# Kernel tuning notes

Hardware: AMD Instinct MI355X
Metric: run time of the kernel (lower is better)

The kernel has to match this reference:

```python
import jax, jax.numpy as jnp
import numpy as np

B = 1024       # batch of graphs
NUM = 512      # predicates / nodes per graph
D = 64         # embedding_dim
H = 64         # hidden_dim
E = 4096       # edges per graph (shared structure across batch)
MAIN_NUM = 10  # softmax segment [0, MAIN_NUM); sigmoid on the rest


def setup_inputs() -> dict:
    key = jax.random.key(0)
    ks = jax.random.split(key, 8)
    x = jax.random.uniform(ks[0], (B, NUM), dtype=jnp.float32)
    embedding = jax.random.normal(ks[1], (NUM, D), dtype=jnp.float32) * 0.1
    W1 = jax.random.normal(ks[2], (D, H), dtype=jnp.float32) * (1.0 / np.sqrt(D))
    b1 = jnp.zeros((H,), jnp.float32)
    W2 = jax.random.normal(ks[3], (H, H), dtype=jnp.float32) * (1.0 / np.sqrt(H))
    b2 = jnp.zeros((H,), jnp.float32)
    W3 = jax.random.normal(ks[4], (H, 1), dtype=jnp.float32) * (1.0 / np.sqrt(H))
    b3 = jnp.zeros((1,), jnp.float32)
    edge_row = jax.random.randint(ks[5], (E,), 0, NUM, dtype=jnp.int32)
    edge_col = jax.random.randint(ks[6], (E,), 0, NUM, dtype=jnp.int32)
    return {"x": x, "embedding": embedding, "W1": W1, "b1": b1,
            "W2": W2, "b2": b2, "W3": W3, "b3": b3,
            "edge_row": edge_row, "edge_col": edge_col}


def _gcn_layer(h, W, b, row, col, norm):
    # h: [B, NUM, in]; GCNConv = linear -> D^{-1/2} A D^{-1/2} aggregate -> +bias
    hW = jnp.einsum('bni,io->bno', h, W)                 # [B, NUM, out]
    msg = hW[:, row, :] * norm[None, :, None]            # [B, E, out]
    agg = jnp.zeros_like(hW).at[:, col, :].add(msg)      # scatter to targets
    return agg + b


def reference(x, embedding, W1, b1, W2, b2, W3, b3, edge_row, edge_col):
    num = x.shape[1]
    # symmetric GCN normalization (add_self_loops=False, unit edge weights)
    deg = jnp.zeros((num,), x.dtype).at[edge_col].add(1.0)
    dinv = jnp.where(deg > 0, jax.lax.rsqrt(jnp.maximum(deg, 1.0)), 0.0)
    norm = dinv[edge_row] * dinv[edge_col]               # [E]

    h = x[..., None] * embedding                         # [B, NUM, D]
    h = jax.nn.relu(_gcn_layer(h, W1, b1, edge_row, edge_col, norm))
    h = jax.nn.relu(_gcn_layer(h, W2, b2, edge_row, edge_col, norm))
    logits = _gcn_layer(h, W3, b3, edge_row, edge_col, norm)[..., 0]  # [B, NUM]

    # convert_to_confidence: softmax over multiclass segment, sigmoid elsewhere
    phi_sm = jax.nn.softmax(logits[:, :MAIN_NUM], axis=1)
    phi_sg = jax.nn.sigmoid(logits[:, MAIN_NUM:])
    return jnp.concatenate([phi_sm, phi_sg], axis=1)
```

## Files before the change

kernel.cpp:

```cpp
#include <hip/hip_runtime.h>
#include <stdint.h>

#define NB    1024
#define NUM   512
#define HD    64
#define NE    4096
#define NEP   4608
#define MAIN  10
#define HBS   72

typedef __attribute__((ext_vector_type(8))) short short8;
typedef __attribute__((ext_vector_type(4))) float f32x4;

__device__ __forceinline__ short f2bf(float f) {
    uint32_t u = __float_as_uint(f);
    u += 0x7fffu + ((u >> 16) & 1u);
    return (short)(u >> 16);
}
__device__ __forceinline__ float bf2f(short s) {
    return __uint_as_float(((uint32_t)(uint16_t)s) << 16);
}

__global__ __launch_bounds__(512) void prep_all(
    const int* __restrict__ erow, const int* __restrict__ ecol,
    const float* __restrict__ emb, const float* __restrict__ W1,
    const float* __restrict__ W2,
    int* __restrict__ rsptr, int* __restrict__ colmap, int* __restrict__ epk,
    short* __restrict__ E1, short* __restrict__ W2T)
{
    const int t = threadIdx.x;
    if (blockIdx.x != 0) {
        int g = (blockIdx.x - 1) * 512 + t;
        if (g < NUM * HD) {
            int node = g >> 6, dim = g & 63;
            float acc = 0.0f;
            #pragma unroll
            for (int k = 0; k < HD; ++k) acc += emb[node * HD + k] * W1[k * HD + dim];
            E1[g] = f2bf(acc);
        } else if (g < NUM * HD + HD * HD) {
            int j = g - NUM * HD;
            int dout = j >> 6, din = j & 63;
            W2T[j] = f2bf(W2[din * HD + dout]);
        }
        return;
    }

    __shared__ int   sdeg[NUM];
    __shared__ int   aux[NUM];
    __shared__ float sdv[NUM];
    __shared__ int   rnk[NUM];
    __shared__ int   rdg[NUM];
    __shared__ int   wsum[8];

    const int lane = t & 63, wv = t >> 6;

    sdeg[t] = 0; aux[t] = 0;
    __syncthreads();
    for (int e = t; e < NE; e += 512) atomicAdd(&sdeg[ecol[e]], 1);
    __syncthreads();
    const int deg  = sdeg[t];
    const int pdeg = (deg + 1) & ~1;
    const int dbin = deg < NUM ? deg : NUM - 1;
    sdv[t] = deg > 0 ? rsqrtf((float)deg) : 0.0f;
    atomicAdd(&aux[dbin], 1);
    __syncthreads();
    {
        int v = aux[t];
        #pragma unroll
        for (int ofs = 1; ofs < 64; ofs <<= 1) {
            int sh = __shfl_up(v, ofs, 64);
            if (lane >= ofs) v += sh;
        }
        if (lane == 63) wsum[wv] = v;
        __syncthreads();
        if (t == 0) {
            int s = 0;
            #pragma unroll
            for (int w = 0; w < 8; ++w) { int tmp = wsum[w]; wsum[w] = s; s += tmp; }
        }
        __syncthreads();
        int inc = v + wsum[wv];
        sdeg[t] = inc - ((dbin == t) ? 0 : 0);
        aux[t]  = inc;
        __syncthreads();
        sdeg[t] = (t == 0) ? 0 : aux[t - 1];
        __syncthreads();
    }
    {
        int r = atomicAdd(&sdeg[dbin], 1);
        rnk[t] = r;
        rdg[r] = pdeg;
        colmap[r] = t;
    }
    __syncthreads();
    {
        int dv = rdg[t], v = dv;
        #pragma unroll
        for (int ofs = 1; ofs < 64; ofs <<= 1) {
            int sh = __shfl_up(v, ofs, 64);
            if (lane >= ofs) v += sh;
        }
        if (lane == 63) wsum[wv] = v;
        __syncthreads();
        if (t == 0) {
            int s = 0;
            #pragma unroll
            for (int w = 0; w < 8; ++w) { int tmp = wsum[w]; wsum[w] = s; s += tmp; }
        }
        __syncthreads();
        int inc  = v + wsum[wv];
        int excl = inc - dv;
        rsptr[t] = excl;
        if (t == NUM - 1) rsptr[NUM] = inc;
        aux[t] = excl;
        __syncthreads();
    }
    sdeg[t] = aux[rnk[t]];
    __syncthreads();
    for (int i = t; i < NEP; i += 512) epk[i] = 0;
    __syncthreads();
    for (int e = t; e < NE; e += 512) {
        int c = ecol[e], rr = erow[e];
        int p = atomicAdd(&sdeg[c], 1);
        unsigned nb = (unsigned short)f2bf(sdv[rr] * sdv[c]);
        epk[p] = (rr << 16) | (int)nb;
    }
}

__global__ __launch_bounds__(1024, 4) void gcn_body(
    const float* __restrict__ x, const short* __restrict__ E1,
    const short* __restrict__ W2T,
    const float* __restrict__ b1, const float* __restrict__ b2,
    const float* __restrict__ W3, const float* __restrict__ b3,
    const int* __restrict__ rsptrg, const int* __restrict__ colmap,
    const int* __restrict__ epkg,
    float* __restrict__ out)
{
    __shared__ short HA[NUM * HD];
    __shared__ short HB[NUM * HBS];
    __shared__ int   eps[NEP];
    __shared__ int   sptr[513];
    __shared__ float sred[2];

    float* tv   = (float*)HB;
    float* slog = ((float*)HB) + NUM;

    const int t     = threadIdx.x;
    const int b     = blockIdx.x;
    const int lane  = t & 63;
    const int wave  = t >> 6;
    const int q     = lane >> 4;
    const int l15   = lane & 15;
    const int grp   = lane >> 3;
    const int dbase = (lane & 7) * 8;

    {
        const int4* g4 = (const int4*)epkg;
        *(int4*)&eps[t * 4] = g4[t];
        if (t < 128) *(int4*)&eps[4096 + t * 4] = g4[1024 + t];
    }
    if (t < 513) sptr[t] = rsptrg[t];

    #pragma unroll
    for (int p = 0; p < 4; ++p) {
        int i = t + p * 1024;
        int r = i >> 3, d8 = (i & 7) * 8;
        float xr = x[b * NUM + r];
        short8 e = *(const short8*)&E1[r * HD + d8];
        short8 o;
        #pragma unroll
        for (int j = 0; j < 8; ++j) o[j] = f2bf(xr * bf2f(e[j]));
        *(short8*)&HA[r * HD + d8] = o;
    }

    float b1v[8], b2v[8], w3v[8];
    {
        f32x4 u0 = *(const f32x4*)&b1[dbase], u1 = *(const f32x4*)&b1[dbase + 4];
        f32x4 v0 = *(const f32x4*)&b2[dbase], v1 = *(const f32x4*)&b2[dbase + 4];
        f32x4 w0 = *(const f32x4*)&W3[dbase], w1 = *(const f32x4*)&W3[dbase + 4];
        #pragma unroll
        for (int j = 0; j < 4; ++j) {
            b1v[j] = u0[j]; b1v[j + 4] = u1[j];
            b2v[j] = v0[j]; b2v[j + 4] = v1[j];
            w3v[j] = w0[j]; w3v[j + 4] = w1[j];
        }
    }
    __syncthreads();

#define EDGE_MAC(pe)                                                          \
    {                                                                         \
        float n = __uint_as_float((unsigned)(pe) << 16);                      \
        uint4 hv = *(const uint4*)&HA[((unsigned)(pe) >> 16) * HD + dbase];   \
        a[0] = fmaf(n, __uint_as_float(hv.x << 16), a[0]);                    \
        a[1] = fmaf(n, __uint_as_float(hv.x), a[1]);                          \
        a[2] = fmaf(n, __uint_as_float(hv.y << 16), a[2]);                    \
        a[3] = fmaf(n, __uint_as_float(hv.y), a[3]);                          \
        a[4] = fmaf(n, __uint_as_float(hv.z << 16), a[4]);                    \
        a[5] = fmaf(n, __uint_as_float(hv.z), a[5]);                          \
        a[6] = fmaf(n, __uint_as_float(hv.w << 16), a[6]);                    \
        a[7] = fmaf(n, __uint_as_float(hv.w), a[7]);                          \
    }

    #pragma unroll 1
    for (int set = 0; set < 4; ++set) {
        int r  = set * 128 + wave * 8 + grp;
        int e0 = sptr[r], e1 = sptr[r + 1];
        int c  = colmap[r];
        float a[8];
        #pragma unroll
        for (int j = 0; j < 8; ++j) a[j] = 0.0f;
        int e = e0;
        for (; e + 4 <= e1; e += 4) {
            int2 pa = *(const int2*)&eps[e];
            int2 pb = *(const int2*)&eps[e + 2];
            EDGE_MAC(pa.x); EDGE_MAC(pa.y); EDGE_MAC(pb.x); EDGE_MAC(pb.y);
        }
        if (e < e1) {
            int2 pa = *(const int2*)&eps[e];
            EDGE_MAC(pa.x); EDGE_MAC(pa.y);
        }
        short8 o;
        #pragma unroll
        for (int j = 0; j < 8; ++j) o[j] = f2bf(fmaxf(a[j] + b1v[j], 0.0f));
        *(short8*)&HB[c * HBS + dbase] = o;
    }
    __syncthreads();

    {
        short8 bfr[2][4];
        #pragma unroll
        for (int ks = 0; ks < 2; ++ks)
            #pragma unroll
            for (int nt = 0; nt < 4; ++nt)
                bfr[ks][nt] = *(const short8*)&W2T[(nt * 16 + l15) * HD + ks * 32 + q * 8];
        f32x4 acc[2][4];
        #pragma unroll
        for (int mt = 0; mt < 2; ++mt)
            #pragma unroll
            for (int nt = 0; nt < 4; ++nt) acc[mt][nt] = (f32x4){0.f, 0.f, 0.f, 0.f};
        const int mbase = wave * 32;
        #pragma unroll
        for (int mt = 0; mt < 2; ++mt)
            #pragma unroll
            for (int ks = 0; ks < 2; ++ks) {
                short8 af = *(const short8*)&HB[(mbase + mt * 16 + l15) * HBS
                                                + ks * 32 + q * 8];
                #pragma unroll
                for (int nt = 0; nt < 4; ++nt)
                    acc[mt][nt] = __builtin_amdgcn_mfma_f32_16x16x32_bf16(
                        af, bfr[ks][nt], acc[mt][nt], 0, 0, 0);
            }
        #pragma unroll
        for (int mt = 0; mt < 2; ++mt)
            #pragma unroll
            for (int nt = 0; nt < 4; ++nt)
                #pragma unroll
                for (int i = 0; i < 4; ++i)
                    HA[(mbase + mt * 16 + q * 4 + i) * HD + nt * 16 + l15] =
                        f2bf(acc[mt][nt][i]);
    }
    __syncthreads();

    #pragma unroll 1
    for (int set = 0; set < 4; ++set) {
        int r  = set * 128 + wave * 8 + grp;
        int e0 = sptr[r], e1 = sptr[r + 1];
        int c  = colmap[r];
        float a[8];
        #pragma unroll
        for (int j = 0; j < 8; ++j) a[j] = 0.0f;
        int e = e0;
        for (; e + 4 <= e1; e += 4) {
            int2 pa = *(const int2*)&eps[e];
            int2 pb = *(const int2*)&eps[e + 2];
            EDGE_MAC(pa.x); EDGE_MAC(pa.y); EDGE_MAC(pb.x); EDGE_MAC(pb.y);
        }
        if (e < e1) {
            int2 pa = *(const int2*)&eps[e];
            EDGE_MAC(pa.x); EDGE_MAC(pa.y);
        }
        float v = 0.0f;
        #pragma unroll
        for (int j = 0; j < 8; ++j)
            v += fmaxf(a[j] + b2v[j], 0.0f) * w3v[j];
        v += __shfl_xor(v, 1, 64);
        v += __shfl_xor(v, 2, 64);
        v += __shfl_xor(v, 4, 64);
        if ((lane & 7) == 0) tv[c] = v;
    }
    __syncthreads();

    if (t < NUM) {
        int e0 = sptr[t], e1 = sptr[t + 1];
        float a = 0.0f;
        for (int e = e0; e < e1; ++e) {
            unsigned pe = (unsigned)eps[e];
            a = fmaf(__uint_as_float(pe << 16), tv[pe >> 16], a);
        }
        slog[colmap[t]] = a + b3[0];
    }
    __syncthreads();

    if (t < 64) {
        float v = (t < MAIN) ? slog[t] : -1e30f;
        float m = v;
        m = fmaxf(m, __shfl_xor(m, 1, 64));
        m = fmaxf(m, __shfl_xor(m, 2, 64));
        m = fmaxf(m, __shfl_xor(m, 4, 64));
        m = fmaxf(m, __shfl_xor(m, 8, 64));
        float ev = (t < MAIN) ? __expf(v - m) : 0.0f;
        ev += __shfl_xor(ev, 1, 64);
        ev += __shfl_xor(ev, 2, 64);
        ev += __shfl_xor(ev, 4, 64);
        ev += __shfl_xor(ev, 8, 64);
        if (t == 0) { sred[0] = m; sred[1] = ev; }
    }
    __syncthreads();

    if (t < NUM) {
        float l = slog[t];
        float o = (t < MAIN) ? __expf(l - sred[0]) / sred[1]
                             : 1.0f / (1.0f + __expf(-l));
        out[b * NUM + t] = o;
    }
#undef EDGE_MAC
}

extern "C" void kernel_launch(void* const* d_in, const int* in_sizes, int n_in,
                              void* d_out, int out_size, void* d_ws, size_t ws_size,
                              hipStream_t stream) {
    const float* x    = (const float*)d_in[0];
    const float* emb  = (const float*)d_in[1];
    const float* W1   = (const float*)d_in[2];
    const float* b1   = (const float*)d_in[3];
    const float* W2   = (const float*)d_in[4];
    const float* b2   = (const float*)d_in[5];
    const float* W3   = (const float*)d_in[6];
    const float* b3   = (const float*)d_in[7];
    const int*   erow = (const int*)d_in[8];
    const int*   ecol = (const int*)d_in[9];

    char* ws = (char*)d_ws;
    int*   rsptr  = (int*)ws;
    int*   colmap = (int*)(ws + 2176);
    int*   epk    = (int*)(ws + 4224);
    short* E1     = (short*)(ws + 22656);
    short* W2T    = (short*)(ws + 88192);

    prep_all<<<73, 512, 0, stream>>>(erow, ecol, emb, W1, W2,
                                     rsptr, colmap, epk, E1, W2T);
    gcn_body<<<NB, 1024, 0, stream>>>(x, E1, W2T, b1, b2, W3, b3,
                                      rsptr, colmap, epk, (float*)d_out);
}
```

Baseline: 157.3 us.

## Switch bf16 to fp16 storage, pre-shift edge indices, unroll gathers, split final aggregation

Changes intermediate storage and MFMA inputs from bf16 to fp16, and packs each edge's source row as a pre-scaled byte offset so the gather address needs only a shift. The edge-gather loops are unrolled to eight edges, with all row loads issued before the FMAs to raise LDS memory-level parallelism. The final scalar aggregation now uses two threads per node with a shuffle reduction. The fp16 conversions use round-toward-zero packing, which trades some accuracy and range for cheaper conversion. Some redundant prep code is also removed.

```diff
diff --git a/kernel.cpp b/kernel.cpp
--- a/kernel.cpp
+++ b/kernel.cpp
@@ -9,16 +9,14 @@
 #define MAIN  10
 #define HBS   72
 
-typedef __attribute__((ext_vector_type(8))) short short8;
+typedef _Float16 hlf;
+typedef __attribute__((ext_vector_type(2))) _Float16 hlf2;
+typedef __attribute__((ext_vector_type(8))) _Float16 hlf8;
 typedef __attribute__((ext_vector_type(4))) float f32x4;
 
-__device__ __forceinline__ short f2bf(float f) {
-    uint32_t u = __float_as_uint(f);
-    u += 0x7fffu + ((u >> 16) & 1u);
-    return (short)(u >> 16);
-}
-__device__ __forceinline__ float bf2f(short s) {
-    return __uint_as_float(((uint32_t)(uint16_t)s) << 16);
+__device__ __forceinline__ unsigned short f2h(float f) {
+    hlf v = (hlf)f;
+    return __builtin_bit_cast(unsigned short, v);
 }
 
 __global__ __launch_bounds__(512) void prep_all(
@@ -36,11 +34,11 @@
             float acc = 0.0f;
             #pragma unroll
             for (int k = 0; k < HD; ++k) acc += emb[node * HD + k] * W1[k * HD + dim];
-            E1[g] = f2bf(acc);
+            E1[g] = (short)f2h(acc);
         } else if (g < NUM * HD + HD * HD) {
             int j = g - NUM * HD;
             int dout = j >> 6, din = j & 63;
-            W2T[j] = f2bf(W2[din * HD + dout]);
+            W2T[j] = (short)f2h(W2[din * HD + dout]);
         }
         return;
     }
@@ -80,7 +78,6 @@
         }
         __syncthreads();
         int inc = v + wsum[wv];
-        sdeg[t] = inc - ((dbin == t) ? 0 : 0);
         aux[t]  = inc;
         __syncthreads();
         sdeg[t] = (t == 0) ? 0 : aux[t - 1];
@@ -108,7 +105,8 @@
             for (int w = 0; w < 8; ++w) { int tmp = wsum[w]; wsum[w] = s; s += tmp; }
         }
         __syncthreads();
-        int inc  = v + wsum[wv];
+        int inc  = v + dv ? (v + wsum[wv]) : (v + wsum[wv]);
+        inc = v + wsum[wv];
         int excl = inc - dv;
         rsptr[t] = excl;
         if (t == NUM - 1) rsptr[NUM] = inc;
@@ -122,24 +120,24 @@
     for (int e = t; e < NE; e += 512) {
         int c = ecol[e], rr = erow[e];
         int p = atomicAdd(&sdeg[c], 1);
-        unsigned nb = (unsigned short)f2bf(sdv[rr] * sdv[c]);
-        epk[p] = (rr << 16) | (int)nb;
+        unsigned ns = (unsigned)f2h(sdv[rr] * sdv[c]);
+        epk[p] = (rr << 23) | (int)ns;
     }
 }
 
 __global__ __launch_bounds__(1024, 4) void gcn_body(
-    const float* __restrict__ x, const short* __restrict__ E1,
-    const short* __restrict__ W2T,
+    const float* __restrict__ x, const hlf* __restrict__ E1,
+    const hlf* __restrict__ W2T,
     const float* __restrict__ b1, const float* __restrict__ b2,
     const float* __restrict__ W3, const float* __restrict__ b3,
     const int* __restrict__ rsptrg, const int* __restrict__ colmap,
     const int* __restrict__ epkg,
     float* __restrict__ out)
 {
-    __shared__ short HA[NUM * HD];
-    __shared__ short HB[NUM * HBS];
-    __shared__ int   eps[NEP];
-    __shared__ int   sptr[513];
+    __shared__ hlf HA[NUM * HD];
+    __shared__ hlf HB[NUM * HBS];
+    __shared__ int eps[NEP];
+    __shared__ int sptr[513];
     __shared__ float sred[2];
 
     float* tv   = (float*)HB;
@@ -166,11 +164,12 @@
         int i = t + p * 1024;
         int r = i >> 3, d8 = (i & 7) * 8;
         float xr = x[b * NUM + r];
-        short8 e = *(const short8*)&E1[r * HD + d8];
-        short8 o;
-        #pragma unroll
-        for (int j = 0; j < 8; ++j) o[j] = f2bf(xr * bf2f(e[j]));
-        *(short8*)&HA[r * HD + d8] = o;
+        hlf  xh = (hlf)xr;
+        hlf8 e  = *(const hlf8*)&E1[r * HD + d8];
+        hlf8 o;
+        #pragma unroll
+        for (int j = 0; j < 8; ++j) o[j] = e[j] * xh;
+        *(hlf8*)&HA[r * HD + d8] = o;
     }
 
     float b1v[8], b2v[8], w3v[8];
@@ -185,21 +184,43 @@
             w3v[j] = w0[j]; w3v[j + 4] = w1[j];
         }
     }
-    __syncthreads();
-
-#define EDGE_MAC(pe)                                                          \
-    {                                                                         \
-        float n = __uint_as_float((unsigned)(pe) << 16);                      \
-        uint4 hv = *(const uint4*)&HA[((unsigned)(pe) >> 16) * HD + dbase];   \
-        a[0] = fmaf(n, __uint_as_float(hv.x << 16), a[0]);                    \
-        a[1] = fmaf(n, __uint_as_float(hv.x), a[1]);                          \
-        a[2] = fmaf(n, __uint_as_float(hv.y << 16), a[2]);                    \
-        a[3] = fmaf(n, __uint_as_float(hv.y), a[3]);                          \
-        a[4] = fmaf(n, __uint_as_float(hv.z << 16), a[4]);                    \
-        a[5] = fmaf(n, __uint_as_float(hv.z), a[5]);                          \
-        a[6] = fmaf(n, __uint_as_float(hv.w << 16), a[6]);                    \
-        a[7] = fmaf(n, __uint_as_float(hv.w), a[7]);                          \
-    }
+    const char* HAb = (const char*)HA + dbase * 2;
+    __syncthreads();
+
+#define LDROW(d, pe) d = *(const uint4*)(HAb + ((unsigned)(pe) >> 16));
+#define MACROW(hv, pe) {                                                      \
+        const hlf nh = __builtin_bit_cast(hlf2, (unsigned)(pe))[0];           \
+        const hlf2 p0 = __builtin_bit_cast(hlf2, (hv).x);                     \
+        const hlf2 p1 = __builtin_bit_cast(hlf2, (hv).y);                     \
+        const hlf2 p2 = __builtin_bit_cast(hlf2, (hv).z);                     \
+        const hlf2 p3 = __builtin_bit_cast(hlf2, (hv).w);                     \
+        a[0] = fmaf((float)p0[0], (float)nh, a[0]);                           \
+        a[1] = fmaf((float)p0[1], (float)nh, a[1]);                           \
+        a[2] = fmaf((float)p1[0], (float)nh, a[2]);                           \
+        a[3] = fmaf((float)p1[1], (float)nh, a[3]);                           \
+        a[4] = fmaf((float)p2[0], (float)nh, a[4]);                           \
+        a[5] = fmaf((float)p2[1], (float)nh, a[5]);                           \
+        a[6] = fmaf((float)p3[0], (float)nh, a[6]);                           \
+        a[7] = fmaf((float)p3[1], (float)nh, a[7]); }
+
+#define CHUNK8 {                                                              \
+        int2 qa = *(const int2*)&eps[e];     int2 qb = *(const int2*)&eps[e + 2]; \
+        int2 qc = *(const int2*)&eps[e + 4]; int2 qd = *(const int2*)&eps[e + 6]; \
+        uint4 v0, v1, v2, v3, v4, v5, v6, v7;                                 \
+        LDROW(v0, qa.x) LDROW(v1, qa.y) LDROW(v2, qb.x) LDROW(v3, qb.y)       \
+        LDROW(v4, qc.x) LDROW(v5, qc.y) LDROW(v6, qd.x) LDROW(v7, qd.y)       \
+        MACROW(v0, qa.x) MACROW(v1, qa.y) MACROW(v2, qb.x) MACROW(v3, qb.y)   \
+        MACROW(v4, qc.x) MACROW(v5, qc.y) MACROW(v6, qd.x) MACROW(v7, qd.y) }
+#define CHUNK4 {                                                              \
+        int2 qa = *(const int2*)&eps[e];     int2 qb = *(const int2*)&eps[e + 2]; \
+        uint4 v0, v1, v2, v3;                                                 \
+        LDROW(v0, qa.x) LDROW(v1, qa.y) LDROW(v2, qb.x) LDROW(v3, qb.y)       \
+        MACROW(v0, qa.x) MACROW(v1, qa.y) MACROW(v2, qb.x) MACROW(v3, qb.y) }
+#define CHUNK2 {                                                              \
+        int2 qa = *(const int2*)&eps[e];                                      \
+        uint4 v0, v1;                                                         \
+        LDROW(v0, qa.x) LDROW(v1, qa.y)                                       \
+        MACROW(v0, qa.x) MACROW(v1, qa.y) }
 
     #pragma unroll 1
     for (int set = 0; set < 4; ++set) {
@@ -210,29 +231,29 @@
         #pragma unroll
         for (int j = 0; j < 8; ++j) a[j] = 0.0f;
         int e = e0;
-        for (; e + 4 <= e1; e += 4) {
-            int2 pa = *(const int2*)&eps[e];
-            int2 pb = *(const int2*)&eps[e + 2];
-            EDGE_MAC(pa.x); EDGE_MAC(pa.y); EDGE_MAC(pb.x); EDGE_MAC(pb.y);
-        }
-        if (e < e1) {
-            int2 pa = *(const int2*)&eps[e];
-            EDGE_MAC(pa.x); EDGE_MAC(pa.y);
-        }
-        short8 o;
-        #pragma unroll
-        for (int j = 0; j < 8; ++j) o[j] = f2bf(fmaxf(a[j] + b1v[j], 0.0f));
-        *(short8*)&HB[c * HBS + dbase] = o;
-    }
-    __syncthreads();
-
-    {
-        short8 bfr[2][4];
+        for (; e + 8 <= e1; e += 8) CHUNK8;
+        if (e + 4 <= e1) { CHUNK4; e += 4; }
+        if (e < e1) CHUNK2;
+        uint4 ov;
+        ov.x = __builtin_bit_cast(unsigned, __builtin_amdgcn_cvt_pkrtz(
+                   fmaxf(a[0] + b1v[0], 0.0f), fmaxf(a[1] + b1v[1], 0.0f)));
+        ov.y = __builtin_bit_cast(unsigned, __builtin_amdgcn_cvt_pkrtz(
+                   fmaxf(a[2] + b1v[2], 0.0f), fmaxf(a[3] + b1v[3], 0.0f)));
+        ov.z = __builtin_bit_cast(unsigned, __builtin_amdgcn_cvt_pkrtz(
+                   fmaxf(a[4] + b1v[4], 0.0f), fmaxf(a[5] + b1v[5], 0.0f)));
+        ov.w = __builtin_bit_cast(unsigned, __builtin_amdgcn_cvt_pkrtz(
+                   fmaxf(a[6] + b1v[6], 0.0f), fmaxf(a[7] + b1v[7], 0.0f)));
+        *(uint4*)&HB[c * HBS + dbase] = ov;
+    }
+    __syncthreads();
+
+    {
+        hlf8 bfr[2][4];
         #pragma unroll
         for (int ks = 0; ks < 2; ++ks)
             #pragma unroll
             for (int nt = 0; nt < 4; ++nt)
-                bfr[ks][nt] = *(const short8*)&W2T[(nt * 16 + l15) * HD + ks * 32 + q * 8];
+                bfr[ks][nt] = *(const hlf8*)&W2T[(nt * 16 + l15) * HD + ks * 32 + q * 8];
         f32x4 acc[2][4];
         #pragma unroll
         for (int mt = 0; mt < 2; ++mt)
@@ -243,11 +264,11 @@
         for (int mt = 0; mt < 2; ++mt)
             #pragma unroll
             for (int ks = 0; ks < 2; ++ks) {
-                short8 af = *(const short8*)&HB[(mbase + mt * 16 + l15) * HBS
-                                                + ks * 32 + q * 8];
+                hlf8 af = *(const hlf8*)&HB[(mbase + mt * 16 + l15) * HBS
+                                            + ks * 32 + q * 8];
                 #pragma unroll
                 for (int nt = 0; nt < 4; ++nt)
-                    acc[mt][nt] = __builtin_amdgcn_mfma_f32_16x16x32_bf16(
+                    acc[mt][nt] = __builtin_amdgcn_mfma_f32_16x16x32_f16(
                         af, bfr[ks][nt], acc[mt][nt], 0, 0, 0);
             }
         #pragma unroll
@@ -257,7 +278,7 @@
                 #pragma unroll
                 for (int i = 0; i < 4; ++i)
                     HA[(mbase + mt * 16 + q * 4 + i) * HD + nt * 16 + l15] =
-                        f2bf(acc[mt][nt][i]);
+                        (hlf)acc[mt][nt][i];
     }
     __syncthreads();
 
@@ -270,15 +291,9 @@
         #pragma unroll
         for (int j = 0; j < 8; ++j) a[j] = 0.0f;
         int e = e0;
-        for (; e + 4 <= e1; e += 4) {
-            int2 pa = *(const int2*)&eps[e];
-            int2 pb = *(const int2*)&eps[e + 2];
-            EDGE_MAC(pa.x); EDGE_MAC(pa.y); EDGE_MAC(pb.x); EDGE_MAC(pb.y);
-        }
-        if (e < e1) {
-            int2 pa = *(const int2*)&eps[e];
-            EDGE_MAC(pa.x); EDGE_MAC(pa.y);
-        }
+        for (; e + 8 <= e1; e += 8) CHUNK8;
+        if (e + 4 <= e1) { CHUNK4; e += 4; }
+        if (e < e1) CHUNK2;
         float v = 0.0f;
         #pragma unroll
         for (int j = 0; j < 8; ++j)
@@ -290,14 +305,20 @@
     }
     __syncthreads();
 
-    if (t < NUM) {
-        int e0 = sptr[t], e1 = sptr[t + 1];
-        float a = 0.0f;
-        for (int e = e0; e < e1; ++e) {
+    {
+        int rk = t >> 1, hh = t & 1;
+        int e0 = sptr[rk], e1 = sptr[rk + 1];
+        int mid = (e0 + e1) >> 1;
+        int ea = hh ? mid : e0;
+        int eb = hh ? e1 : mid;
+        float acc = 0.0f;
+        for (int e = ea; e < eb; ++e) {
             unsigned pe = (unsigned)eps[e];
-            a = fmaf(__uint_as_float(pe << 16), tv[pe >> 16], a);
-        }
-        slog[colmap[t]] = a + b3[0];
+            float nf = (float)__builtin_bit_cast(hlf2, pe)[0];
+            acc = fmaf(nf, *(const float*)((const char*)tv + (pe >> 21)), acc);
+        }
+        acc += __shfl_xor(acc, 1, 64);
+        if (!hh) slog[colmap[rk]] = acc + b3[0];
     }
     __syncthreads();
 
@@ -323,7 +344,11 @@
                              : 1.0f / (1.0f + __expf(-l));
         out[b * NUM + t] = o;
     }
-#undef EDGE_MAC
+#undef LDROW
+#undef MACROW
+#undef CHUNK8
+#undef CHUNK4
+#undef CHUNK2
 }
 
 extern "C" void kernel_launch(void* const* d_in, const int* in_sizes, int n_in,
@@ -349,6 +374,7 @@
 
     prep_all<<<73, 512, 0, stream>>>(erow, ecol, emb, W1, W2,
                                      rsptr, colmap, epk, E1, W2T);
-    gcn_body<<<NB, 1024, 0, stream>>>(x, E1, W2T, b1, b2, W3, b3,
+    gcn_body<<<NB, 1024, 0, stream>>>(x, (const hlf*)E1, (const hlf*)W2T,
+                                      b1, b2, W3, b3,
                                       rsptr, colmap, epk, (float*)d_out);
 }
```

Result: no change. 155.4 us (-1.2%).
